# Kernel optimization log

Hardware: AMD Instinct MI355X
Metric: run time of the kernel (lower is better)

The kernel has to match this reference:

```python
import jax, jax.numpy as jnp
import numpy as np

B, C_IN, H, W = 8, 32, 64, 64
C = 64  # num_channels


def setup_inputs() -> dict:
    key = jax.random.key(0)
    ks = jax.random.split(key, 9)
    s_in = 1.0 / np.sqrt(C_IN)
    s_c = 1.0 / np.sqrt(C)
    return {
        "x": jax.random.normal(ks[0], (B, C_IN, H, W), dtype=jnp.float32),
        "wq": jax.random.uniform(ks[1], (C, C_IN), jnp.float32, -s_in, s_in),
        "bq": jax.random.uniform(ks[2], (C,), jnp.float32, -s_in, s_in),
        "wk": jax.random.uniform(ks[3], (C, C_IN), jnp.float32, -s_in, s_in),
        "bk": jax.random.uniform(ks[4], (C,), jnp.float32, -s_in, s_in),
        "wv": jax.random.uniform(ks[5], (C, C_IN), jnp.float32, -s_in, s_in),
        "bv": jax.random.uniform(ks[6], (C,), jnp.float32, -s_in, s_in),
        "wo": jax.random.uniform(ks[7], (C_IN, C), jnp.float32, -s_c, s_c),
        "bo": jax.random.uniform(ks[8], (C_IN,), jnp.float32, -s_c, s_c),
    }


def reference(x, wq, bq, wk, bk, wv, bv, wo, bo):
    b, c_in, h, w = x.shape
    n = h * w
    # 1x1 convs == per-pixel linear projections; produce (B, N, C) directly
    q = (jnp.einsum('bchw,oc->bhwo', x, wq) + bq).reshape(b, n, -1)
    k = (jnp.einsum('bchw,oc->bhwo', x, wk) + bk).reshape(b, n, -1)
    v = (jnp.einsum('bchw,oc->bhwo', x, wv) + bv).reshape(b, n, -1)
    # unscaled attention over spatial positions (no 1/sqrt(d) in original)
    scores = jnp.einsum('bnc,bmc->bnm', q, k)  # (B, N, N)
    attn = jax.nn.softmax(scores, axis=-1)
    out = jnp.einsum('bnm,bmc->bnc', attn, v)  # (B, N, C)
    out = out.reshape(b, h, w, -1)
    out = jnp.einsum('bhwc,oc->bohw', out, wo) + bo[None, :, None, None]
    return out + x
```

## Files before the change

kernel.cpp:

```cpp
#include <hip/hip_runtime.h>
#include <hip/hip_bf16.h>

#define CIN    32
#define NPIX   4096
#define DIM    64
#define LOG2E  1.4426950408889634f

#if __has_builtin(__builtin_amdgcn_exp2f)
#define EXP2(x) __builtin_amdgcn_exp2f(x)
#else
#define EXP2(x) exp2f(x)
#endif

typedef float  f32x4 __attribute__((ext_vector_type(4)));
typedef short  s16x8 __attribute__((ext_vector_type(8)));

__device__ __forceinline__ unsigned short bf16_bits(float f) {
    union { __hip_bfloat16 h; unsigned short u; } cv;
    cv.h = __float2bfloat16(f);
    return cv.u;
}


__global__ __launch_bounds__(256) void qkv_proj(
    const float* __restrict__ x,
    const float* __restrict__ wq, const float* __restrict__ bq,
    const float* __restrict__ wk, const float* __restrict__ bk,
    const float* __restrict__ wv, const float* __restrict__ bv,
    __hip_bfloat16* __restrict__ qb, __hip_bfloat16* __restrict__ kb,
    __hip_bfloat16* __restrict__ vb)
{
    __shared__ float Xs[CIN][64];
    __shared__ float wT[3][CIN][DIM];

    const int tid = threadIdx.x;
    const int b   = blockIdx.y;
    const int bx  = blockIdx.x;
    const int n0  = bx * 64;

    for (int i = tid; i < 3 * CIN * DIM; i += 256) {
        int m = i >> 11, r = i & 2047, c = r >> 6, o = r & 63;
        const float* wsrc = (m == 0) ? wq : (m == 1) ? wk : wv;
        float wv0 = wsrc[o * CIN + c];
        wT[m][c][o] = (m == 0) ? wv0 * LOG2E : wv0;
    }
    for (int i = tid * 4; i < CIN * 64; i += 1024) {
        int c = i >> 6, p = i & 63;
        *(f32x4*)&Xs[c][p] = *(const f32x4*)&x[((size_t)b * CIN + c) * NPIX + n0 + p];
    }
    __syncthreads();

    const int w    = tid >> 6;
    const int lane = tid & 63;
    const int l16  = lane >> 2;
    const int quad = lane & 3;

    const int T  = bx * 4 + w;
    const int px = T * 16 + l16;

    float aq[2][8], ak[2][8];
    #pragma unroll
    for (int kb2 = 0; kb2 < 2; kb2++) {
        f32x4 bq0 = *(const f32x4*)&bq[kb2 * 32 + quad * 8];
        f32x4 bq1 = *(const f32x4*)&bq[kb2 * 32 + quad * 8 + 4];
        f32x4 bk0 = *(const f32x4*)&bk[kb2 * 32 + quad * 8];
        f32x4 bk1 = *(const f32x4*)&bk[kb2 * 32 + quad * 8 + 4];
        #pragma unroll
        for (int j = 0; j < 4; j++) {
            aq[kb2][j] = bq0[j] * LOG2E; aq[kb2][j + 4] = bq1[j] * LOG2E;
            ak[kb2][j] = bk0[j];         ak[kb2][j + 4] = bk1[j];
        }
    }
    #pragma unroll 8
    for (int c = 0; c < CIN; c++) {
        const float xc = Xs[c][w * 16 + l16];
        #pragma unroll
        for (int kb2 = 0; kb2 < 2; kb2++) {
            f32x4 q0 = *(const f32x4*)&wT[0][c][kb2 * 32 + quad * 8];
            f32x4 q1 = *(const f32x4*)&wT[0][c][kb2 * 32 + quad * 8 + 4];
            f32x4 k0 = *(const f32x4*)&wT[1][c][kb2 * 32 + quad * 8];
            f32x4 k1 = *(const f32x4*)&wT[1][c][kb2 * 32 + quad * 8 + 4];
            #pragma unroll
            for (int j = 0; j < 4; j++) {
                aq[kb2][j]     += xc * q0[j];
                aq[kb2][j + 4] += xc * q1[j];
                ak[kb2][j]     += xc * k0[j];
                ak[kb2][j + 4] += xc * k1[j];
            }
        }
    }
    #pragma unroll
    for (int kb2 = 0; kb2 < 2; kb2++) {
        union { s16x8 v; __hip_bfloat16 h[8]; } pq, pk;
        #pragma unroll
        for (int j = 0; j < 8; j++) {
            pq.h[j] = __float2bfloat16(aq[kb2][j]);
            pk.h[j] = __float2bfloat16(ak[kb2][j]);
        }
        *(s16x8*)(qb + ((size_t)b * NPIX + px) * DIM + kb2 * 32 + quad * 8) = pq.v;
        const size_t koff =
            ((((size_t)(b * 256 + T) * 2 + kb2) * 16 + l16) * 4 + quad) * 8;
        *(s16x8*)(kb + koff) = pk.v;
    }

    const int ch = w * 16 + l16;
    float av[2][8];
    {
        const float bvc = bv[ch];
        #pragma unroll
        for (int kh = 0; kh < 2; kh++)
            #pragma unroll
            for (int j = 0; j < 8; j++) av[kh][j] = bvc;
    }
    #pragma unroll 8
    for (int c = 0; c < CIN; c++) {
        const float wvc = wT[2][c][ch];
        f32x4 x0 = *(const f32x4*)&Xs[c][quad * 8];
        f32x4 x1 = *(const f32x4*)&Xs[c][quad * 8 + 4];
        f32x4 x2 = *(const f32x4*)&Xs[c][32 + quad * 8];
        f32x4 x3 = *(const f32x4*)&Xs[c][32 + quad * 8 + 4];
        #pragma unroll
        for (int j = 0; j < 4; j++) {
            av[0][j]     += x0[j] * wvc;
            av[0][j + 4] += x1[j] * wvc;
            av[1][j]     += x2[j] * wvc;
            av[1][j + 4] += x3[j] * wvc;
        }
    }
    #pragma unroll
    for (int kh = 0; kh < 2; kh++) {
        union { s16x8 v; __hip_bfloat16 h[8]; } pv;
        #pragma unroll
        for (int j = 0; j < 8; j++) pv.h[j] = __float2bfloat16(av[kh][j]);
        const size_t voff =
            (((((size_t)(b * 64 + bx) * 2 + kh) * 4 + w) * 16 + l16) * 4 + quad) * 8;
        *(s16x8*)(vb + voff) = pv.v;
    }
}

#define PM_OFF   0
#define RED_OFF  0
#define LRED_OFF 50688
#define ON_OFF   51456
#define SMEM_SZ  60672

__global__ __launch_bounds__(256, 2) void attn_fused(
    const __hip_bfloat16* __restrict__ qb,
    const __hip_bfloat16* __restrict__ kbf,
    const __hip_bfloat16* __restrict__ vbf,
    const float* __restrict__ wo, const float* __restrict__ bo,
    const float* __restrict__ x, float* __restrict__ y)
{
    __shared__ __align__(16) char smem[SMEM_SZ];

    const int tid  = threadIdx.x;
    const int kq   = tid >> 6;
    const int lane = tid & 63;
    const int quad = lane >> 4, l16 = lane & 15;
    const int b    = blockIdx.x;
    const int row0 = blockIdx.y * 64;

    s16x8 qf[4][2];
    #pragma unroll
    for (int mt = 0; mt < 4; mt++)
        #pragma unroll
        for (int kb2 = 0; kb2 < 2; kb2++)
            qf[mt][kb2] = *(const s16x8*)(qb
                + ((size_t)b * NPIX + row0 + mt * 16 + l16) * DIM + kb2 * 32 + quad * 8);

    const f32x4 zero4 = {0.f, 0.f, 0.f, 0.f};
    f32x4 o[4][4];
    #pragma unroll
    for (int mt = 0; mt < 4; mt++)
        #pragma unroll
        for (int ct = 0; ct < 4; ct++) o[mt][ct] = zero4;
    f32x4 ol[4] = {zero4, zero4, zero4, zero4};

    s16x8 ones;
    #pragma unroll
    for (int j = 0; j < 8; j++) ones[j] = (short)0x3F80;

    const char* kp = (const char*)kbf + (size_t)b * 524288 + kq * 131072
                     + (l16 * 4 + quad) * 16;
    const char* vp = (const char*)vbf + (size_t)b * 524288 + kq * 131072
                     + (l16 * 4 + quad) * 16;
    char* pmw = smem + PM_OFF + kq * 4608;

    s16x8 ckA[4], cvA[4], ckB[4], cvB[4];
    #pragma unroll
    for (int i = 0; i < 4; i++) {
        ckA[i] = *(const s16x8*)(kp + i * 1024);
        cvA[i] = *(const s16x8*)(vp + i * 1024);
    }

    auto step = [&](s16x8 (&curK)[4], s16x8 (&curV)[4],
                    s16x8 (&nxtK)[4], s16x8 (&nxtV)[4]) {
        kp += 4096; vp += 4096;
        f32x4 st[2][4];
        #pragma unroll
        for (int nt = 0; nt < 2; nt++)
            #pragma unroll
            for (int mt = 0; mt < 4; mt++) {
                st[nt][mt] = __builtin_amdgcn_mfma_f32_16x16x32_bf16(
                    curK[nt * 2 + 0], qf[mt][0], zero4, 0, 0, 0);
                st[nt][mt] = __builtin_amdgcn_mfma_f32_16x16x32_bf16(
                    curK[nt * 2 + 1], qf[mt][1], st[nt][mt], 0, 0, 0);
            }
        #pragma unroll
        for (int i = 0; i < 4; i++) nxtK[i] = *(const s16x8*)(kp + i * 1024);

        #pragma unroll
        for (int nt = 0; nt < 2; nt++)
            #pragma unroll
            for (int mt = 0; mt < 4; mt++) {
                f32x4 p = st[nt][mt];
                #pragma unroll
                for (int r = 0; r < 4; r++) p[r] = EXP2(p[r]);
                unsigned int d0 = (__float_as_uint(p[1]) & 0xffff0000u)
                                | (__float_as_uint(p[0]) >> 16);
                unsigned int d1 = (__float_as_uint(p[3]) & 0xffff0000u)
                                | (__float_as_uint(p[2]) >> 16);
                unsigned long long dd = ((unsigned long long)d1 << 32) | d0;
                *(unsigned long long*)(pmw + (mt * 16 + l16) * 72 + nt * 32 + quad * 8) = dd;
            }
        s16x8 pf[4];
        #pragma unroll
        for (int mt = 0; mt < 4; mt++)
            pf[mt] = *(const s16x8*)(pmw + (mt * 16 + l16) * 72 + quad * 16);

        #pragma unroll
        for (int ct = 0; ct < 4; ct++)
            #pragma unroll
            for (int mt = 0; mt < 4; mt++)
                o[mt][ct] = __builtin_amdgcn_mfma_f32_16x16x32_bf16(
                    pf[mt], curV[ct], o[mt][ct], 0, 0, 0);
        #pragma unroll
        for (int mt = 0; mt < 4; mt++)
            ol[mt] = __builtin_amdgcn_mfma_f32_16x16x32_bf16(
                pf[mt], ones, ol[mt], 0, 0, 0);
        #pragma unroll
        for (int i = 0; i < 4; i++) nxtV[i] = *(const s16x8*)(vp + i * 1024);
    };

    for (int it = 0; it < 16; it++) {
        step(ckA, cvA, ckB, cvB);
        step(ckB, cvB, ckA, cvA);
    }

    __syncthreads();

    float* RED  = (float*)(smem + RED_OFF);
    float* LRED = (float*)(smem + LRED_OFF);

    if (kq != 0) {
        float* R = RED + (kq - 1) * 64 * 66;
        float* L = LRED + (kq - 1) * 64;
        #pragma unroll
        for (int mt = 0; mt < 4; mt++) {
            #pragma unroll
            for (int ct = 0; ct < 4; ct++)
                #pragma unroll
                for (int r = 0; r < 4; r++)
                    R[(mt * 16 + quad * 4 + r) * 66 + ct * 16 + l16] = o[mt][ct][r];
            if (l16 == 0)
                #pragma unroll
                for (int r = 0; r < 4; r++)
                    L[mt * 16 + quad * 4 + r] = ol[mt][r];
        }
    }
    __syncthreads();

    if (kq == 0) {
        #pragma unroll
        for (int reg = 0; reg < 3; reg++) {
            const float* R = RED + reg * 64 * 66;
            const float* L = LRED + reg * 64;
            #pragma unroll
            for (int mt = 0; mt < 4; mt++)
                #pragma unroll
                for (int r = 0; r < 4; r++) {
                    ol[mt][r] += L[mt * 16 + quad * 4 + r];
                    #pragma unroll
                    for (int ct = 0; ct < 4; ct++)
                        o[mt][ct][r] += R[(mt * 16 + quad * 4 + r) * 66 + ct * 16 + l16];
                }
        }

        __hip_bfloat16* ON = (__hip_bfloat16*)(smem + ON_OFF);
        #pragma unroll
        for (int mt = 0; mt < 4; mt++)
            #pragma unroll
            for (int r = 0; r < 4; r++) {
                const float inv = 1.0f / ol[mt][r];
                #pragma unroll
                for (int ct = 0; ct < 4; ct++)
                    ON[(mt * 16 + quad * 4 + r) * 72 + ct * 16 + l16]
                        = __float2bfloat16(o[mt][ct][r] * inv);
            }
        s16x8 af[4][2];
        #pragma unroll
        for (int mt = 0; mt < 4; mt++)
            #pragma unroll
            for (int kb2 = 0; kb2 < 2; kb2++)
                af[mt][kb2] = *(const s16x8*)(ON + (mt * 16 + l16) * 72
                                              + kb2 * 32 + quad * 8);

        f32x4 d[4][2];
        #pragma unroll
        for (int mt = 0; mt < 4; mt++)
            #pragma unroll
            for (int nt = 0; nt < 2; nt++) d[mt][nt] = zero4;
        #pragma unroll
        for (int nt = 0; nt < 2; nt++)
            #pragma unroll
            for (int kb2 = 0; kb2 < 2; kb2++) {
                const float* wp = wo + (size_t)(nt * 16 + l16) * DIM + kb2 * 32 + quad * 8;
                union { s16x8 v; __hip_bfloat16 h[8]; } wf;
                #pragma unroll
                for (int j = 0; j < 8; j++) wf.h[j] = __float2bfloat16(wp[j]);
                #pragma unroll
                for (int mt = 0; mt < 4; mt++)
                    d[mt][nt] = __builtin_amdgcn_mfma_f32_16x16x32_bf16(
                        af[mt][kb2], wf.v, d[mt][nt], 0, 0, 0);
            }

        #pragma unroll
        for (int nt = 0; nt < 2; nt++) {
            const int out = nt * 16 + l16;
            const float bias = bo[out];
            #pragma unroll
            for (int mt = 0; mt < 4; mt++)
                #pragma unroll
                for (int r = 0; r < 4; r++) {
                    const int row = row0 + mt * 16 + quad * 4 + r;
                    const size_t xi = ((size_t)b * CIN + out) * NPIX + row;
                    y[xi] = d[mt][nt][r] + bias + x[xi];
                }
        }
    }
}

extern "C" void kernel_launch(void* const* d_in, const int* in_sizes, int n_in,
                              void* d_out, int out_size, void* d_ws, size_t ws_size,
                              hipStream_t stream)
{
    const float* x  = (const float*)d_in[0];
    const float* wq = (const float*)d_in[1];
    const float* bq = (const float*)d_in[2];
    const float* wk = (const float*)d_in[3];
    const float* bk = (const float*)d_in[4];
    const float* wv = (const float*)d_in[5];
    const float* bv = (const float*)d_in[6];
    const float* wo = (const float*)d_in[7];
    const float* bo = (const float*)d_in[8];
    float* y = (float*)d_out;

    char* ws = (char*)d_ws;
    __hip_bfloat16* qb = (__hip_bfloat16*)(ws);
    __hip_bfloat16* kb = (__hip_bfloat16*)(ws + (4u << 20));
    __hip_bfloat16* vb = (__hip_bfloat16*)(ws + (8u << 20));

    qkv_proj<<<dim3(64, 8), dim3(256), 0, stream>>>(x, wq, bq, wk, bk, wv, bv, qb, kb, vb);
    attn_fused<<<dim3(8, 64), dim3(256), 0, stream>>>(qb, kb, vb, wo, bo, x, y);
}
```

Measured before the change: 134.1 us.

## Feed softmax probabilities to PV MFMA directly from registers using 16x16x16 ops

Computes P·V as the transposed product (V^T·P^T) using 16x16x16 bf16 MFMAs. The exp'd score accumulator layout then serves directly as the B operand, which removes the LDS round trip for P. V is stored by the projection kernel in a new interleaved layout to match the new operand order. The epilogue is reworked in the same transposed form, which removes the LDS staging of the normalized output before the Wo projection. In exchange it issues twice as many smaller MFMA instructions, which may have lower throughput per FLOP than the 16x16x32 variant.

```diff
diff --git a/kernel.cpp b/kernel.cpp
--- a/kernel.cpp
+++ b/kernel.cpp
@@ -14,11 +14,18 @@
 
 typedef float  f32x4 __attribute__((ext_vector_type(4)));
 typedef short  s16x8 __attribute__((ext_vector_type(8)));
-
-__device__ __forceinline__ unsigned short bf16_bits(float f) {
-    union { __hip_bfloat16 h; unsigned short u; } cv;
-    cv.h = __float2bfloat16(f);
-    return cv.u;
+typedef short  s16x4 __attribute__((ext_vector_type(4)));
+
+__device__ __forceinline__ f32x4 mfma16(s16x4 a, s16x4 b, f32x4 c) {
+#if __has_builtin(__builtin_amdgcn_mfma_f32_16x16x16bf16_1k)
+    return __builtin_amdgcn_mfma_f32_16x16x16bf16_1k(a, b, c, 0, 0, 0);
+#elif __has_builtin(__builtin_amdgcn_mfma_f32_16x16x16_bf16)
+    return __builtin_amdgcn_mfma_f32_16x16x16_bf16(a, b, c, 0, 0, 0);
+#else
+    f32x4 d;
+    asm("v_mfma_f32_16x16x16_bf16 %0, %1, %2, %3" : "=v"(d) : "v"(a), "v"(b), "v"(c));
+    return d;
+#endif
 }
 
 
@@ -129,20 +136,18 @@
     }
     #pragma unroll
     for (int kh = 0; kh < 2; kh++) {
-        union { s16x8 v; __hip_bfloat16 h[8]; } pv;
-        #pragma unroll
-        for (int j = 0; j < 8; j++) pv.h[j] = __float2bfloat16(av[kh][j]);
-        const size_t voff =
-            (((((size_t)(b * 64 + bx) * 2 + kh) * 4 + w) * 16 + l16) * 4 + quad) * 8;
-        *(s16x8*)(vb + voff) = pv.v;
+        #pragma unroll
+        for (int h = 0; h < 2; h++) {
+            union { unsigned long long u; __hip_bfloat16 hh[4]; } pv;
+            #pragma unroll
+            for (int j = 0; j < 4; j++) pv.hh[j] = __float2bfloat16(av[kh][h * 4 + j]);
+            const int lanep = ((quad & 1) * 2 + h) * 16 + l16;
+            const size_t chunk =
+                (((size_t)(b * 128 + bx * 2 + kh) * 4 + w) * 64 + lanep) * 2 + (quad >> 1);
+            *(unsigned long long*)(vb + chunk * 4) = pv.u;
+        }
     }
 }
-
-#define PM_OFF   0
-#define RED_OFF  0
-#define LRED_OFF 50688
-#define ON_OFF   51456
-#define SMEM_SZ  60672
 
 __global__ __launch_bounds__(256, 2) void attn_fused(
     const __hip_bfloat16* __restrict__ qb,
@@ -151,7 +156,8 @@
     const float* __restrict__ wo, const float* __restrict__ bo,
     const float* __restrict__ x, float* __restrict__ y)
 {
-    __shared__ __align__(16) char smem[SMEM_SZ];
+    __shared__ __align__(16) float RED[3][64][66];
+    __shared__ float LRED[3][64];
 
     const int tid  = threadIdx.x;
     const int kq   = tid >> 6;
@@ -176,15 +182,14 @@
         for (int ct = 0; ct < 4; ct++) o[mt][ct] = zero4;
     f32x4 ol[4] = {zero4, zero4, zero4, zero4};
 
-    s16x8 ones;
-    #pragma unroll
-    for (int j = 0; j < 8; j++) ones[j] = (short)0x3F80;
+    s16x4 ones;
+    #pragma unroll
+    for (int j = 0; j < 4; j++) ones[j] = (short)0x3F80;
 
     const char* kp = (const char*)kbf + (size_t)b * 524288 + kq * 131072
                      + (l16 * 4 + quad) * 16;
     const char* vp = (const char*)vbf + (size_t)b * 524288 + kq * 131072
-                     + (l16 * 4 + quad) * 16;
-    char* pmw = smem + PM_OFF + kq * 4608;
+                     + lane * 16;
 
     s16x8 ckA[4], cvA[4], ckB[4], cvB[4];
     #pragma unroll
@@ -209,6 +214,7 @@
         #pragma unroll
         for (int i = 0; i < 4; i++) nxtK[i] = *(const s16x8*)(kp + i * 1024);
 
+        s16x4 pb[2][4];
         #pragma unroll
         for (int nt = 0; nt < 2; nt++)
             #pragma unroll
@@ -216,28 +222,29 @@
                 f32x4 p = st[nt][mt];
                 #pragma unroll
                 for (int r = 0; r < 4; r++) p[r] = EXP2(p[r]);
-                unsigned int d0 = (__float_as_uint(p[1]) & 0xffff0000u)
-                                | (__float_as_uint(p[0]) >> 16);
-                unsigned int d1 = (__float_as_uint(p[3]) & 0xffff0000u)
-                                | (__float_as_uint(p[2]) >> 16);
-                unsigned long long dd = ((unsigned long long)d1 << 32) | d0;
-                *(unsigned long long*)(pmw + (mt * 16 + l16) * 72 + nt * 32 + quad * 8) = dd;
-            }
-        s16x8 pf[4];
-        #pragma unroll
-        for (int mt = 0; mt < 4; mt++)
-            pf[mt] = *(const s16x8*)(pmw + (mt * 16 + l16) * 72 + quad * 16);
-
-        #pragma unroll
-        for (int ct = 0; ct < 4; ct++)
-            #pragma unroll
-            for (int mt = 0; mt < 4; mt++)
-                o[mt][ct] = __builtin_amdgcn_mfma_f32_16x16x32_bf16(
-                    pf[mt], curV[ct], o[mt][ct], 0, 0, 0);
-        #pragma unroll
-        for (int mt = 0; mt < 4; mt++)
-            ol[mt] = __builtin_amdgcn_mfma_f32_16x16x32_bf16(
-                pf[mt], ones, ol[mt], 0, 0, 0);
+                union { unsigned int d[2]; s16x4 v; } pk;
+                pk.d[0] = (__float_as_uint(p[1]) & 0xffff0000u)
+                        | (__float_as_uint(p[0]) >> 16);
+                pk.d[1] = (__float_as_uint(p[3]) & 0xffff0000u)
+                        | (__float_as_uint(p[2]) >> 16);
+                pb[nt][mt] = pk.v;
+            }
+
+        #pragma unroll
+        for (int ct = 0; ct < 4; ct++) {
+            s16x4 vlo = __builtin_shufflevector(curV[ct], curV[ct], 0, 1, 2, 3);
+            s16x4 vhi = __builtin_shufflevector(curV[ct], curV[ct], 4, 5, 6, 7);
+            #pragma unroll
+            for (int mt = 0; mt < 4; mt++) {
+                o[mt][ct] = mfma16(vlo, pb[0][mt], o[mt][ct]);
+                o[mt][ct] = mfma16(vhi, pb[1][mt], o[mt][ct]);
+            }
+        }
+        #pragma unroll
+        for (int mt = 0; mt < 4; mt++) {
+            ol[mt] = mfma16(ones, pb[0][mt], ol[mt]);
+            ol[mt] = mfma16(ones, pb[1][mt], ol[mt]);
+        }
         #pragma unroll
         for (int i = 0; i < 4; i++) nxtV[i] = *(const s16x8*)(vp + i * 1024);
     };
@@ -247,96 +254,86 @@
         step(ckB, cvB, ckA, cvA);
     }
 
+    if (kq != 0) {
+        #pragma unroll
+        for (int mt = 0; mt < 4; mt++) {
+            #pragma unroll
+            for (int ct = 0; ct < 4; ct++)
+                #pragma unroll
+                for (int r = 0; r < 4; r++)
+                    RED[kq - 1][ct * 16 + quad * 4 + r][mt * 16 + l16] = o[mt][ct][r];
+            if (quad == 0)
+                LRED[kq - 1][mt * 16 + l16] = ol[mt][0];
+        }
+    }
     __syncthreads();
 
-    float* RED  = (float*)(smem + RED_OFF);
-    float* LRED = (float*)(smem + LRED_OFF);
-
-    if (kq != 0) {
-        float* R = RED + (kq - 1) * 64 * 66;
-        float* L = LRED + (kq - 1) * 64;
+    if (kq == 0) {
+        #pragma unroll
+        for (int reg = 0; reg < 3; reg++)
+            #pragma unroll
+            for (int mt = 0; mt < 4; mt++) {
+                ol[mt][0] += LRED[reg][mt * 16 + l16];
+                #pragma unroll
+                for (int ct = 0; ct < 4; ct++)
+                    #pragma unroll
+                    for (int r = 0; r < 4; r++)
+                        o[mt][ct][r] += RED[reg][ct * 16 + quad * 4 + r][mt * 16 + l16];
+            }
+
+        s16x4 pvo[4][4];
         #pragma unroll
         for (int mt = 0; mt < 4; mt++) {
-            #pragma unroll
-            for (int ct = 0; ct < 4; ct++)
+            const float inv = 1.0f / ol[mt][0];
+            #pragma unroll
+            for (int ct = 0; ct < 4; ct++) {
+                union { s16x4 v; __hip_bfloat16 h[4]; } pk;
                 #pragma unroll
                 for (int r = 0; r < 4; r++)
-                    R[(mt * 16 + quad * 4 + r) * 66 + ct * 16 + l16] = o[mt][ct][r];
-            if (l16 == 0)
-                #pragma unroll
-                for (int r = 0; r < 4; r++)
-                    L[mt * 16 + quad * 4 + r] = ol[mt][r];
-        }
-    }
-    __syncthreads();
-
-    if (kq == 0) {
-        #pragma unroll
-        for (int reg = 0; reg < 3; reg++) {
-            const float* R = RED + reg * 64 * 66;
-            const float* L = LRED + reg * 64;
-            #pragma unroll
-            for (int mt = 0; mt < 4; mt++)
-                #pragma unroll
-                for (int r = 0; r < 4; r++) {
-                    ol[mt][r] += L[mt * 16 + quad * 4 + r];
-                    #pragma unroll
-                    for (int ct = 0; ct < 4; ct++)
-                        o[mt][ct][r] += R[(mt * 16 + quad * 4 + r) * 66 + ct * 16 + l16];
+                    pk.h[r] = __float2bfloat16(o[mt][ct][r] * inv);
+                pvo[mt][ct] = pk.v;
+            }
+        }
+
+        s16x4 aw[2][4];
+        #pragma unroll
+        for (int nt = 0; nt < 2; nt++)
+            #pragma unroll
+            for (int ct = 0; ct < 4; ct++) {
+                f32x4 w4 = *(const f32x4*)(wo + (size_t)(nt * 16 + l16) * DIM
+                                           + ct * 16 + quad * 4);
+                union { s16x4 v; __hip_bfloat16 h[4]; } wf;
+                #pragma unroll
+                for (int j = 0; j < 4; j++) wf.h[j] = __float2bfloat16(w4[j]);
+                aw[nt][ct] = wf.v;
+            }
+
+        f32x4 d2[4][2];
+        #pragma unroll
+        for (int mt = 0; mt < 4; mt++)
+            #pragma unroll
+            for (int nt = 0; nt < 2; nt++) d2[mt][nt] = zero4;
+        #pragma unroll
+        for (int ct = 0; ct < 4; ct++)
+            #pragma unroll
+            for (int nt = 0; nt < 2; nt++)
+                #pragma unroll
+                for (int mt = 0; mt < 4; mt++)
+                    d2[mt][nt] = mfma16(aw[nt][ct], pvo[mt][ct], d2[mt][nt]);
+
+        #pragma unroll
+        for (int nt = 0; nt < 2; nt++)
+            #pragma unroll
+            for (int r = 0; r < 4; r++) {
+                const int out = nt * 16 + quad * 4 + r;
+                const float bias = bo[out];
+                #pragma unroll
+                for (int mt = 0; mt < 4; mt++) {
+                    const int row = row0 + mt * 16 + l16;
+                    const size_t xi = ((size_t)b * CIN + out) * NPIX + row;
+                    y[xi] = d2[mt][nt][r] + bias + x[xi];
                 }
-        }
-
-        __hip_bfloat16* ON = (__hip_bfloat16*)(smem + ON_OFF);
-        #pragma unroll
-        for (int mt = 0; mt < 4; mt++)
-            #pragma unroll
-            for (int r = 0; r < 4; r++) {
-                const float inv = 1.0f / ol[mt][r];
-                #pragma unroll
-                for (int ct = 0; ct < 4; ct++)
-                    ON[(mt * 16 + quad * 4 + r) * 72 + ct * 16 + l16]
-                        = __float2bfloat16(o[mt][ct][r] * inv);
-            }
-        s16x8 af[4][2];
-        #pragma unroll
-        for (int mt = 0; mt < 4; mt++)
-            #pragma unroll
-            for (int kb2 = 0; kb2 < 2; kb2++)
-                af[mt][kb2] = *(const s16x8*)(ON + (mt * 16 + l16) * 72
-                                              + kb2 * 32 + quad * 8);
-
-        f32x4 d[4][2];
-        #pragma unroll
-        for (int mt = 0; mt < 4; mt++)
-            #pragma unroll
-            for (int nt = 0; nt < 2; nt++) d[mt][nt] = zero4;
-        #pragma unroll
-        for (int nt = 0; nt < 2; nt++)
-            #pragma unroll
-            for (int kb2 = 0; kb2 < 2; kb2++) {
-                const float* wp = wo + (size_t)(nt * 16 + l16) * DIM + kb2 * 32 + quad * 8;
-                union { s16x8 v; __hip_bfloat16 h[8]; } wf;
-                #pragma unroll
-                for (int j = 0; j < 8; j++) wf.h[j] = __float2bfloat16(wp[j]);
-                #pragma unroll
-                for (int mt = 0; mt < 4; mt++)
-                    d[mt][nt] = __builtin_amdgcn_mfma_f32_16x16x32_bf16(
-                        af[mt][kb2], wf.v, d[mt][nt], 0, 0, 0);
-            }
-
-        #pragma unroll
-        for (int nt = 0; nt < 2; nt++) {
-            const int out = nt * 16 + l16;
-            const float bias = bo[out];
-            #pragma unroll
-            for (int mt = 0; mt < 4; mt++)
-                #pragma unroll
-                for (int r = 0; r < 4; r++) {
-                    const int row = row0 + mt * 16 + quad * 4 + r;
-                    const size_t xi = ((size_t)b * CIN + out) * NPIX + row;
-                    y[xi] = d[mt][nt][r] + bias + x[xi];
-                }
-        }
+            }
     }
 }
 
```

New measurement: 132.2 us. No clear change (-1.4%).
